# Kernel optimization log

Measured on AMD Instinct MI355X. Metric: run time of the kernel, lower is better.

## Reference

```python
import jax, jax.numpy as jnp
import numpy as np

B, T, L = 512, 1024, 48


def setup_inputs() -> dict:
    key = jax.random.key(0)
    k_e, k_tr, k_st, k_en = jax.random.split(key, 4)
    emissions = jax.random.normal(k_e, (B, T, L), dtype=jnp.float32)
    mask = jnp.ones((B, T), dtype=bool)  # unused by the original decode body
    transitions = jax.random.normal(k_tr, (L, L), dtype=jnp.float32) * 0.1
    start_transitions = jax.random.normal(k_st, (L,), dtype=jnp.float32) * 0.1
    end_transitions = jax.random.normal(k_en, (L,), dtype=jnp.float32) * 0.1
    return {
        "emissions": emissions,
        "mask": mask,
        "transitions": transitions,
        "start_transitions": start_transitions,
        "end_transitions": end_transitions,
    }


def reference(emissions, mask, transitions, start_transitions, end_transitions):
    # Viterbi forward (max-plus recurrence) over time, vectorized over batch.
    v0 = start_transitions[None, :] + emissions[:, 0]  # [B, L]

    def step(v, e_t):
        # scores[b, i, j] = v[b, i] + transitions[i, j]
        scores = v[:, :, None] + transitions[None, :, :]  # [B, L, L]
        best = jnp.max(scores, axis=1)                    # [B, L]
        bp = jnp.argmax(scores, axis=1).astype(jnp.int32)  # [B, L] best prev tag
        return best + e_t, bp

    em_rest = jnp.moveaxis(emissions[:, 1:], 1, 0)  # [T-1, B, L]
    v_final, bps = jax.lax.scan(step, v0, em_rest)  # bps: [T-1, B, L]
    v_final = v_final + end_transitions[None, :]
    best_last = jnp.argmax(v_final, axis=1).astype(jnp.int32)  # [B]

    # Backtrack: bps[t] maps tag at time t+1 -> best tag at time t.
    def back(tag, bp):
        prev = jnp.take_along_axis(bp, tag[:, None], axis=1)[:, 0]  # [B]
        return prev, prev

    _, tags_0_to_Tm2 = jax.lax.scan(back, best_last, bps, reverse=True)  # [T-1, B]
    paths = jnp.concatenate([tags_0_to_Tm2, best_last[None, :]], axis=0)  # [T, B]
    return paths.T  # [B, T] decoded tag sequences
```

## Files before the change

### kernel.cpp

```cpp
#include <hip/hip_runtime.h>
#include <math.h>

#define BB 512
#define TT 1024
#define LL 48
#define PF 8

__device__ __forceinline__ float readlane_f(float v, int lane) {
    return __int_as_float(__builtin_amdgcn_readlane(__float_as_int(v), lane));
}

__device__ __forceinline__ void argmax48(const float* s, float& bestv, int& besti) {
    float val[24];
    int   idx[24];
#pragma unroll
    for (int k = 0; k < 24; ++k) {
        bool c = s[2 * k + 1] > s[2 * k];
        val[k] = c ? s[2 * k + 1] : s[2 * k];
        idx[k] = c ? 2 * k + 1 : 2 * k;
    }
#pragma unroll
    for (int k = 0; k < 12; ++k) {
        bool c = val[2 * k + 1] > val[2 * k];
        val[k] = c ? val[2 * k + 1] : val[2 * k];
        idx[k] = c ? idx[2 * k + 1] : idx[2 * k];
    }
#pragma unroll
    for (int k = 0; k < 6; ++k) {
        bool c = val[2 * k + 1] > val[2 * k];
        val[k] = c ? val[2 * k + 1] : val[2 * k];
        idx[k] = c ? idx[2 * k + 1] : idx[2 * k];
    }
#pragma unroll
    for (int k = 0; k < 3; ++k) {
        bool c = val[2 * k + 1] > val[2 * k];
        val[k] = c ? val[2 * k + 1] : val[2 * k];
        idx[k] = c ? idx[2 * k + 1] : idx[2 * k];
    }
    bool c01 = val[1] > val[0];
    float bv = c01 ? val[1] : val[0];
    int   bi = c01 ? idx[1] : idx[0];
    bool c2 = val[2] > bv;
    bestv = c2 ? val[2] : bv;
    besti = c2 ? idx[2] : bi;
}

__global__ __launch_bounds__(64) void viterbi_kernel(
    const float* __restrict__ emissions,
    const float* __restrict__ transitions,
    const float* __restrict__ start_tr,
    const float* __restrict__ end_tr,
    int* __restrict__ out)
{
    __shared__ unsigned char bp[(TT - 1) * LL];

    const int b  = blockIdx.x;
    const int j  = threadIdx.x;
    const int jc = (j < LL) ? j : (LL - 1);

    float tc[LL];
#pragma unroll
    for (int i = 0; i < LL; ++i)
        tc[i] = transitions[i * LL + jc];

    const float* em = emissions + (size_t)b * TT * LL;

    float v = start_tr[jc] + em[jc];

    float er[PF];
#pragma unroll
    for (int k = 0; k < PF; ++k)
        er[k] = em[(size_t)(1 + k) * LL + jc];

    auto step = [&](int t, float e) {
        float s[LL];
#pragma unroll
        for (int i = 0; i < LL; ++i)
            s[i] = readlane_f(v, i) + tc[i];

        float m1[16];
#pragma unroll
        for (int k = 0; k < 16; ++k)
            m1[k] = fmaxf(fmaxf(s[3 * k], s[3 * k + 1]), s[3 * k + 2]);
        float m2[6];
#pragma unroll
        for (int k = 0; k < 5; ++k)
            m2[k] = fmaxf(fmaxf(m1[3 * k], m1[3 * k + 1]), m1[3 * k + 2]);
        m2[5] = m1[15];
        float best = fmaxf(fmaxf(fmaxf(m2[0], m2[1]), m2[2]),
                           fmaxf(fmaxf(m2[3], m2[4]), m2[5]));

        v = best + e;

        int i0 = 63, i1 = 63, i2 = 63, i3 = 63;
#pragma unroll
        for (int k = 11; k >= 0; --k) {
            if (s[k]      == best) i0 = k;
            if (s[12 + k] == best) i1 = 12 + k;
            if (s[24 + k] == best) i2 = 24 + k;
            if (s[36 + k] == best) i3 = 36 + k;
        }
        int arg = min(min(i0, i1), min(i2, i3));

        bp[(t - 1) * LL + jc] = (unsigned char)arg;
    };

    int tb = 1;
    for (; tb + PF <= TT; tb += PF) {
#pragma unroll
        for (int k = 0; k < PF; ++k) {
            int t = tb + k;
            float e = er[k];
            int tn = t + PF; if (tn > TT - 1) tn = TT - 1;
            er[k] = em[(size_t)tn * LL + jc];
            step(t, e);
        }
    }
#pragma unroll
    for (int k = 0; k < PF - 1; ++k) {
        int t = tb + k;
        if (t < TT) step(t, er[k]);
    }

    v += end_tr[jc];
    float sf[LL];
#pragma unroll
    for (int i = 0; i < LL; ++i)
        sf[i] = readlane_f(v, i);
    float bestv; int tag;
    argmax48(sf, bestv, tag);

    int* ob = out + (size_t)b * TT;
    if (j == 0) ob[TT - 1] = tag;

    for (int hi = TT - 2; hi >= 0; hi -= 32) {
        int lo = hi - 31; if (lo < 0) lo = 0;
        int n = hi - lo + 1;

        unsigned int row[32];
#pragma unroll
        for (int k = 0; k < 32; ++k)
            row[k] = (unsigned int)bp[(lo + k) * LL + jc];

        int outv = 0;
#pragma unroll
        for (int k = 31; k >= 0; --k) {
            if (k < n) {
                tag = __builtin_amdgcn_readlane((int)row[k], tag);
                outv = (j == k) ? tag : outv;
            }
        }
        if (j < n) ob[lo + j] = outv;
    }
}

extern "C" void kernel_launch(void* const* d_in, const int* in_sizes, int n_in,
                              void* d_out, int out_size, void* d_ws, size_t ws_size,
                              hipStream_t stream) {
    const float* emissions   = (const float*)d_in[0];
    const float* transitions = (const float*)d_in[2];
    const float* start_tr    = (const float*)d_in[3];
    const float* end_tr      = (const float*)d_in[4];
    int* out = (int*)d_out;

    viterbi_kernel<<<dim3(BB), dim3(64), 0, stream>>>(
        emissions, transitions, start_tr, end_tr, out);
}
```

Baseline: 572.1 us.

## Process two batch rows per wavefront to interleave independent Viterbi recurrences

Each 64-thread block now decodes two sequences at once, interleaving their max-plus steps and backtracking. The aim is instruction-level parallelism, hiding readlane and dependency latency along the serial time chain. The cost is half as many blocks and twice the instructions per wave. Shared memory for backpointers doubles and is now dynamic, with the max size raised once on the host.

```diff
diff --git a/kernel.cpp b/kernel.cpp
--- a/kernel.cpp
+++ b/kernel.cpp
@@ -45,16 +45,19 @@
     besti = c2 ? idx[2] : bi;
 }
 
-__global__ __launch_bounds__(64) void viterbi_kernel(
+__global__ __launch_bounds__(64, 1) void viterbi_kernel(
     const float* __restrict__ emissions,
     const float* __restrict__ transitions,
     const float* __restrict__ start_tr,
     const float* __restrict__ end_tr,
     int* __restrict__ out)
 {
-    __shared__ unsigned char bp[(TT - 1) * LL];
-
-    const int b  = blockIdx.x;
+    extern __shared__ unsigned char bp[];
+    unsigned char* bpA = bp;
+    unsigned char* bpB = bp + (TT - 1) * LL;
+
+    const int bA = blockIdx.x * 2;
+    const int bB = bA + 1;
     const int j  = threadIdx.x;
     const int jc = (j < LL) ? j : (LL - 1);
 
@@ -63,46 +66,67 @@
     for (int i = 0; i < LL; ++i)
         tc[i] = transitions[i * LL + jc];
 
-    const float* em = emissions + (size_t)b * TT * LL;
-
-    float v = start_tr[jc] + em[jc];
-
-    float er[PF];
-#pragma unroll
-    for (int k = 0; k < PF; ++k)
-        er[k] = em[(size_t)(1 + k) * LL + jc];
-
-    auto step = [&](int t, float e) {
-        float s[LL];
-#pragma unroll
-        for (int i = 0; i < LL; ++i)
-            s[i] = readlane_f(v, i) + tc[i];
-
-        float m1[16];
-#pragma unroll
-        for (int k = 0; k < 16; ++k)
-            m1[k] = fmaxf(fmaxf(s[3 * k], s[3 * k + 1]), s[3 * k + 2]);
-        float m2[6];
-#pragma unroll
-        for (int k = 0; k < 5; ++k)
-            m2[k] = fmaxf(fmaxf(m1[3 * k], m1[3 * k + 1]), m1[3 * k + 2]);
-        m2[5] = m1[15];
-        float best = fmaxf(fmaxf(fmaxf(m2[0], m2[1]), m2[2]),
-                           fmaxf(fmaxf(m2[3], m2[4]), m2[5]));
-
-        v = best + e;
-
-        int i0 = 63, i1 = 63, i2 = 63, i3 = 63;
+    const float* emA = emissions + (size_t)bA * TT * LL;
+    const float* emB = emissions + (size_t)bB * TT * LL;
+
+    float vA = start_tr[jc] + emA[jc];
+    float vB = start_tr[jc] + emB[jc];
+
+    float erA[PF], erB[PF];
+#pragma unroll
+    for (int k = 0; k < PF; ++k) {
+        erA[k] = emA[(size_t)(1 + k) * LL + jc];
+        erB[k] = emB[(size_t)(1 + k) * LL + jc];
+    }
+
+    auto step2 = [&](int t, float eA, float eB) {
+        float sA[LL], sB[LL];
+#pragma unroll
+        for (int i = 0; i < LL; ++i) {
+            sA[i] = readlane_f(vA, i) + tc[i];
+            sB[i] = readlane_f(vB, i) + tc[i];
+        }
+
+        float m1A[16], m1B[16];
+#pragma unroll
+        for (int k = 0; k < 16; ++k) {
+            m1A[k] = fmaxf(fmaxf(sA[3 * k], sA[3 * k + 1]), sA[3 * k + 2]);
+            m1B[k] = fmaxf(fmaxf(sB[3 * k], sB[3 * k + 1]), sB[3 * k + 2]);
+        }
+        float m2A[6], m2B[6];
+#pragma unroll
+        for (int k = 0; k < 5; ++k) {
+            m2A[k] = fmaxf(fmaxf(m1A[3 * k], m1A[3 * k + 1]), m1A[3 * k + 2]);
+            m2B[k] = fmaxf(fmaxf(m1B[3 * k], m1B[3 * k + 1]), m1B[3 * k + 2]);
+        }
+        m2A[5] = m1A[15];
+        m2B[5] = m1B[15];
+        float bestA = fmaxf(fmaxf(fmaxf(m2A[0], m2A[1]), m2A[2]),
+                            fmaxf(fmaxf(m2A[3], m2A[4]), m2A[5]));
+        float bestB = fmaxf(fmaxf(fmaxf(m2B[0], m2B[1]), m2B[2]),
+                            fmaxf(fmaxf(m2B[3], m2B[4]), m2B[5]));
+
+        vA = bestA + eA;
+        vB = bestB + eB;
+
+        int a0 = 63, a1 = 63, a2 = 63, a3 = 63;
+        int b0 = 63, b1 = 63, b2 = 63, b3 = 63;
 #pragma unroll
         for (int k = 11; k >= 0; --k) {
-            if (s[k]      == best) i0 = k;
-            if (s[12 + k] == best) i1 = 12 + k;
-            if (s[24 + k] == best) i2 = 24 + k;
-            if (s[36 + k] == best) i3 = 36 + k;
-        }
-        int arg = min(min(i0, i1), min(i2, i3));
-
-        bp[(t - 1) * LL + jc] = (unsigned char)arg;
+            if (sA[k]      == bestA) a0 = k;
+            if (sA[12 + k] == bestA) a1 = 12 + k;
+            if (sA[24 + k] == bestA) a2 = 24 + k;
+            if (sA[36 + k] == bestA) a3 = 36 + k;
+            if (sB[k]      == bestB) b0 = k;
+            if (sB[12 + k] == bestB) b1 = 12 + k;
+            if (sB[24 + k] == bestB) b2 = 24 + k;
+            if (sB[36 + k] == bestB) b3 = 36 + k;
+        }
+        int argA = min(min(a0, a1), min(a2, a3));
+        int argB = min(min(b0, b1), min(b2, b3));
+
+        bpA[(t - 1) * LL + jc] = (unsigned char)argA;
+        bpB[(t - 1) * LL + jc] = (unsigned char)argB;
     };
 
     int tb = 1;
@@ -110,47 +134,64 @@
 #pragma unroll
         for (int k = 0; k < PF; ++k) {
             int t = tb + k;
-            float e = er[k];
+            float eA = erA[k];
+            float eB = erB[k];
             int tn = t + PF; if (tn > TT - 1) tn = TT - 1;
-            er[k] = em[(size_t)tn * LL + jc];
-            step(t, e);
+            erA[k] = emA[(size_t)tn * LL + jc];
+            erB[k] = emB[(size_t)tn * LL + jc];
+            step2(t, eA, eB);
         }
     }
 #pragma unroll
     for (int k = 0; k < PF - 1; ++k) {
         int t = tb + k;
-        if (t < TT) step(t, er[k]);
-    }
-
-    v += end_tr[jc];
-    float sf[LL];
-#pragma unroll
-    for (int i = 0; i < LL; ++i)
-        sf[i] = readlane_f(v, i);
-    float bestv; int tag;
-    argmax48(sf, bestv, tag);
-
-    int* ob = out + (size_t)b * TT;
-    if (j == 0) ob[TT - 1] = tag;
+        if (t < TT) step2(t, erA[k], erB[k]);
+    }
+
+    vA += end_tr[jc];
+    vB += end_tr[jc];
+    float sfA[LL], sfB[LL];
+#pragma unroll
+    for (int i = 0; i < LL; ++i) {
+        sfA[i] = readlane_f(vA, i);
+        sfB[i] = readlane_f(vB, i);
+    }
+    float bvA, bvB; int tagA, tagB;
+    argmax48(sfA, bvA, tagA);
+    argmax48(sfB, bvB, tagB);
+
+    int* obA = out + (size_t)bA * TT;
+    int* obB = out + (size_t)bB * TT;
+    if (j == 0) {
+        obA[TT - 1] = tagA;
+        obB[TT - 1] = tagB;
+    }
 
     for (int hi = TT - 2; hi >= 0; hi -= 32) {
         int lo = hi - 31; if (lo < 0) lo = 0;
         int n = hi - lo + 1;
 
-        unsigned int row[32];
-#pragma unroll
-        for (int k = 0; k < 32; ++k)
-            row[k] = (unsigned int)bp[(lo + k) * LL + jc];
-
-        int outv = 0;
+        unsigned int rowA[32], rowB[32];
+#pragma unroll
+        for (int k = 0; k < 32; ++k) {
+            rowA[k] = (unsigned int)bpA[(lo + k) * LL + jc];
+            rowB[k] = (unsigned int)bpB[(lo + k) * LL + jc];
+        }
+
+        int outA = 0, outB = 0;
 #pragma unroll
         for (int k = 31; k >= 0; --k) {
             if (k < n) {
-                tag = __builtin_amdgcn_readlane((int)row[k], tag);
-                outv = (j == k) ? tag : outv;
+                tagA = __builtin_amdgcn_readlane((int)rowA[k], tagA);
+                outA = (j == k) ? tagA : outA;
+                tagB = __builtin_amdgcn_readlane((int)rowB[k], tagB);
+                outB = (j == k) ? tagB : outB;
             }
         }
-        if (j < n) ob[lo + j] = outv;
+        if (j < n) {
+            obA[lo + j] = outA;
+            obB[lo + j] = outB;
+        }
     }
 }
 
@@ -163,6 +204,16 @@
     const float* end_tr      = (const float*)d_in[4];
     int* out = (int*)d_out;
 
-    viterbi_kernel<<<dim3(BB), dim3(64), 0, stream>>>(
+    const int lds_bytes = 2 * (TT - 1) * LL;
+
+    static bool attr_set = false;
+    if (!attr_set) {
+        (void)hipFuncSetAttribute((const void*)viterbi_kernel,
+                                  hipFuncAttributeMaxDynamicSharedMemorySize,
+                                  lds_bytes);
+        attr_set = true;
+    }
+
+    viterbi_kernel<<<dim3(BB / 2), dim3(64), lds_bytes, stream>>>(
         emissions, transitions, start_tr, end_tr, out);
 }
```

Result: slower. 1.520 ms (+165.7%).

## Split Viterbi max-plus reduction across two wavefronts with LDS exchange

Applied to the files above, without the earlier changes.

Each block now uses two wavefronts, each handling half of the 48 previous-state candidates per time step. Partial max/argmax values are exchanged through double-buffered shared memory with a barrier each step, and only the first wave writes backpointers and does the backtrack. The goal is to halve the per-step serial readlane and max work on the critical path, at the cost of a workgroup barrier and an LDS round trip every step.

```diff
diff --git a/kernel.cpp b/kernel.cpp
--- a/kernel.cpp
+++ b/kernel.cpp
@@ -5,6 +5,7 @@
 #define TT 1024
 #define LL 48
 #define PF 8
+#define HALF 24
 
 __device__ __forceinline__ float readlane_f(float v, int lane) {
     return __int_as_float(__builtin_amdgcn_readlane(__float_as_int(v), lane));
@@ -45,7 +46,7 @@
     besti = c2 ? idx[2] : bi;
 }
 
-__global__ __launch_bounds__(64) void viterbi_kernel(
+__global__ __launch_bounds__(128) void viterbi_kernel(
     const float* __restrict__ emissions,
     const float* __restrict__ transitions,
     const float* __restrict__ start_tr,
@@ -53,15 +54,19 @@
     int* __restrict__ out)
 {
     __shared__ unsigned char bp[(TT - 1) * LL];
+    __shared__ uint2 xch[2][2][64];
 
-    const int b  = blockIdx.x;
-    const int j  = threadIdx.x;
-    const int jc = (j < LL) ? j : (LL - 1);
+    const int b   = blockIdx.x;
+    const int tid = threadIdx.x;
+    const int w   = tid >> 6;
+    const int j   = tid & 63;
+    const int jc  = (j < LL) ? j : (LL - 1);
+    const int ibase = w * HALF;
 
-    float tc[LL];
+    float tc[HALF];
 #pragma unroll
-    for (int i = 0; i < LL; ++i)
-        tc[i] = transitions[i * LL + jc];
+    for (int i = 0; i < HALF; ++i)
+        tc[i] = transitions[(ibase + i) * LL + jc];
 
     const float* em = emissions + (size_t)b * TT * LL;
 
@@ -72,37 +77,48 @@
     for (int k = 0; k < PF; ++k)
         er[k] = em[(size_t)(1 + k) * LL + jc];
 
-    auto step = [&](int t, float e) {
-        float s[LL];
+    auto step = [&](int t, float e, int parity) {
+        float s[HALF];
 #pragma unroll
-        for (int i = 0; i < LL; ++i)
-            s[i] = readlane_f(v, i) + tc[i];
+        for (int i = 0; i < HALF; ++i)
+            s[i] = readlane_f(v, ibase + i) + tc[i];
 
-        float m1[16];
+        float m1[8];
 #pragma unroll
-        for (int k = 0; k < 16; ++k)
+        for (int k = 0; k < 8; ++k)
             m1[k] = fmaxf(fmaxf(s[3 * k], s[3 * k + 1]), s[3 * k + 2]);
-        float m2[6];
-#pragma unroll
-        for (int k = 0; k < 5; ++k)
-            m2[k] = fmaxf(fmaxf(m1[3 * k], m1[3 * k + 1]), m1[3 * k + 2]);
-        m2[5] = m1[15];
-        float best = fmaxf(fmaxf(fmaxf(m2[0], m2[1]), m2[2]),
-                           fmaxf(fmaxf(m2[3], m2[4]), m2[5]));
+        float mA = fmaxf(fmaxf(m1[0], m1[1]), m1[2]);
+        float mB = fmaxf(fmaxf(m1[3], m1[4]), m1[5]);
+        float mC = fmaxf(m1[6], m1[7]);
+        float best_own = fmaxf(fmaxf(mA, mB), mC);
 
-        v = best + e;
-
-        int i0 = 63, i1 = 63, i2 = 63, i3 = 63;
+        int i0 = 63, i1 = 63;
 #pragma unroll
         for (int k = 11; k >= 0; --k) {
-            if (s[k]      == best) i0 = k;
-            if (s[12 + k] == best) i1 = 12 + k;
-            if (s[24 + k] == best) i2 = 24 + k;
-            if (s[36 + k] == best) i3 = 36 + k;
+            if (s[k]      == best_own) i0 = ibase + k;
+            if (s[12 + k] == best_own) i1 = ibase + 12 + k;
         }
-        int arg = min(min(i0, i1), min(i2, i3));
+        int arg_own = min(i0, i1);
 
-        bp[(t - 1) * LL + jc] = (unsigned char)arg;
+        xch[parity][w][j] = make_uint2(__float_as_uint(best_own), (unsigned)arg_own);
+        asm volatile("s_waitcnt lgkmcnt(0)" ::: "memory");
+        __builtin_amdgcn_s_barrier();
+        uint2 o = xch[parity][w ^ 1][jc];
+        float m_oth = __uint_as_float(o.x);
+        int   a_oth = (int)o.y;
+
+        float m_low  = (w == 0) ? best_own : m_oth;
+        int   a_low  = (w == 0) ? arg_own  : a_oth;
+        float m_high = (w == 0) ? m_oth    : best_own;
+        int   a_high = (w == 0) ? a_oth    : arg_own;
+        bool  hw_    = m_high > m_low;
+        float bestv  = hw_ ? m_high : m_low;
+        int   barg   = hw_ ? a_high : a_low;
+
+        v = bestv + e;
+
+        if (w == 0)
+            bp[(t - 1) * LL + jc] = (unsigned char)barg;
     };
 
     int tb = 1;
@@ -113,44 +129,46 @@
             float e = er[k];
             int tn = t + PF; if (tn > TT - 1) tn = TT - 1;
             er[k] = em[(size_t)tn * LL + jc];
-            step(t, e);
+            step(t, e, (k + 1) & 1);
         }
     }
 #pragma unroll
     for (int k = 0; k < PF - 1; ++k) {
         int t = tb + k;
-        if (t < TT) step(t, er[k]);
+        if (t < TT) step(t, er[k], (k + 1) & 1);
     }
 
-    v += end_tr[jc];
-    float sf[LL];
+    if (w == 0) {
+        float vf = v + end_tr[jc];
+        float sf[LL];
 #pragma unroll
-    for (int i = 0; i < LL; ++i)
-        sf[i] = readlane_f(v, i);
-    float bestv; int tag;
-    argmax48(sf, bestv, tag);
+        for (int i = 0; i < LL; ++i)
+            sf[i] = readlane_f(vf, i);
+        float bestv; int tag;
+        argmax48(sf, bestv, tag);
 
-    int* ob = out + (size_t)b * TT;
-    if (j == 0) ob[TT - 1] = tag;
+        int* ob = out + (size_t)b * TT;
+        if (j == 0) ob[TT - 1] = tag;
 
-    for (int hi = TT - 2; hi >= 0; hi -= 32) {
-        int lo = hi - 31; if (lo < 0) lo = 0;
-        int n = hi - lo + 1;
+        for (int hi = TT - 2; hi >= 0; hi -= 32) {
+            int lo = hi - 31; if (lo < 0) lo = 0;
+            int n = hi - lo + 1;
 
-        unsigned int row[32];
+            unsigned int row[32];
 #pragma unroll
-        for (int k = 0; k < 32; ++k)
-            row[k] = (unsigned int)bp[(lo + k) * LL + jc];
+            for (int k = 0; k < 32; ++k)
+                row[k] = (unsigned int)bp[(lo + k) * LL + jc];
 
-        int outv = 0;
+            int outv = 0;
 #pragma unroll
-        for (int k = 31; k >= 0; --k) {
-            if (k < n) {
-                tag = __builtin_amdgcn_readlane((int)row[k], tag);
-                outv = (j == k) ? tag : outv;
+            for (int k = 31; k >= 0; --k) {
+                if (k < n) {
+                    tag = __builtin_amdgcn_readlane((int)row[k], tag);
+                    outv = (j == k) ? tag : outv;
+                }
             }
+            if (j < n) ob[lo + j] = outv;
         }
-        if (j < n) ob[lo + j] = outv;
     }
 }
 
@@ -163,6 +181,6 @@
     const float* end_tr      = (const float*)d_in[4];
     int* out = (int*)d_out;
 
-    viterbi_kernel<<<dim3(BB), dim3(64), 0, stream>>>(
+    viterbi_kernel<<<dim3(BB), dim3(128), 0, stream>>>(
         emissions, transitions, start_tr, end_tr, out);
 }
```

After: 924.2 us. 61.6% more time.

## Store Viterbi scores to workspace and recompute argmax during backtrack

Applied to the files above, without the earlier changes.

The forward pass no longer computes a per-step argmax backpointer. It only writes the score vector v for each step to a global workspace. The backtrack recomputes each predecessor with a DPP wave-wide max plus a ballot, reading the transition column from LDS. This takes the 48-way equality-scan argmax off the serial forward critical path, at the cost of a 100 MB global write stream and a serial chain of about 1023 wave reductions per sequence during backtrack.

```diff
diff --git a/kernel.cpp b/kernel.cpp
--- a/kernel.cpp
+++ b/kernel.cpp
@@ -5,44 +5,30 @@
 #define TT 1024
 #define LL 48
 #define PF 8
+#define TSTRIDE 49
 
 __device__ __forceinline__ float readlane_f(float v, int lane) {
     return __int_as_float(__builtin_amdgcn_readlane(__float_as_int(v), lane));
 }
 
-__device__ __forceinline__ void argmax48(const float* s, float& bestv, int& besti) {
-    float val[24];
-    int   idx[24];
-#pragma unroll
-    for (int k = 0; k < 24; ++k) {
-        bool c = s[2 * k + 1] > s[2 * k];
-        val[k] = c ? s[2 * k + 1] : s[2 * k];
-        idx[k] = c ? 2 * k + 1 : 2 * k;
-    }
-#pragma unroll
-    for (int k = 0; k < 12; ++k) {
-        bool c = val[2 * k + 1] > val[2 * k];
-        val[k] = c ? val[2 * k + 1] : val[2 * k];
-        idx[k] = c ? idx[2 * k + 1] : idx[2 * k];
-    }
-#pragma unroll
-    for (int k = 0; k < 6; ++k) {
-        bool c = val[2 * k + 1] > val[2 * k];
-        val[k] = c ? val[2 * k + 1] : val[2 * k];
-        idx[k] = c ? idx[2 * k + 1] : idx[2 * k];
-    }
-#pragma unroll
-    for (int k = 0; k < 3; ++k) {
-        bool c = val[2 * k + 1] > val[2 * k];
-        val[k] = c ? val[2 * k + 1] : val[2 * k];
-        idx[k] = c ? idx[2 * k + 1] : idx[2 * k];
-    }
-    bool c01 = val[1] > val[0];
-    float bv = c01 ? val[1] : val[0];
-    int   bi = c01 ? idx[1] : idx[0];
-    bool c2 = val[2] > bv;
-    bestv = c2 ? val[2] : bv;
-    besti = c2 ? idx[2] : bi;
+template <int CTRL>
+__device__ __forceinline__ float dppmax(float x) {
+    int y = __builtin_amdgcn_update_dpp(__float_as_int(x), __float_as_int(x),
+                                        CTRL, 0xF, 0xF, false);
+    return fmaxf(x, __int_as_float(y));
+}
+
+__device__ __forceinline__ int wave_argmax(float z) {
+    float r = z;
+    r = dppmax<0xB1>(r);
+    r = dppmax<0x4E>(r);
+    r = dppmax<0x141>(r);
+    r = dppmax<0x140>(r);
+    r = dppmax<0x142>(r);
+    r = dppmax<0x143>(r);
+    float m = readlane_f(r, 63);
+    unsigned long long eq = __ballot(z == m);
+    return (int)__builtin_ctzll(eq);
 }
 
 __global__ __launch_bounds__(64) void viterbi_kernel(
@@ -50,9 +36,10 @@
     const float* __restrict__ transitions,
     const float* __restrict__ start_tr,
     const float* __restrict__ end_tr,
-    int* __restrict__ out)
+    int* __restrict__ out,
+    float* __restrict__ vws)
 {
-    __shared__ unsigned char bp[(TT - 1) * LL];
+    __shared__ float tlds[LL * TSTRIDE];
 
     const int b  = blockIdx.x;
     const int j  = threadIdx.x;
@@ -60,12 +47,16 @@
 
     float tc[LL];
 #pragma unroll
-    for (int i = 0; i < LL; ++i)
+    for (int i = 0; i < LL; ++i) {
         tc[i] = transitions[i * LL + jc];
+        tlds[i * TSTRIDE + jc] = tc[i];
+    }
 
     const float* em = emissions + (size_t)b * TT * LL;
+    float* vr_g = vws + (size_t)b * TT * LL;
 
     float v = start_tr[jc] + em[jc];
+    vr_g[jc] = v;
 
     float er[PF];
 #pragma unroll
@@ -91,18 +82,7 @@
                            fmaxf(fmaxf(m2[3], m2[4]), m2[5]));
 
         v = best + e;
-
-        int i0 = 63, i1 = 63, i2 = 63, i3 = 63;
-#pragma unroll
-        for (int k = 11; k >= 0; --k) {
-            if (s[k]      == best) i0 = k;
-            if (s[12 + k] == best) i1 = 12 + k;
-            if (s[24 + k] == best) i2 = 24 + k;
-            if (s[36 + k] == best) i3 = 36 + k;
-        }
-        int arg = min(min(i0, i1), min(i2, i3));
-
-        bp[(t - 1) * LL + jc] = (unsigned char)arg;
+        vr_g[(size_t)t * LL + jc] = v;
     };
 
     int tb = 1;
@@ -122,13 +102,8 @@
         if (t < TT) step(t, er[k]);
     }
 
-    v += end_tr[jc];
-    float sf[LL];
-#pragma unroll
-    for (int i = 0; i < LL; ++i)
-        sf[i] = readlane_f(v, i);
-    float bestv; int tag;
-    argmax48(sf, bestv, tag);
+    float vf = (j < LL) ? (v + end_tr[jc]) : -INFINITY;
+    int tag = wave_argmax(vf);
 
     int* ob = out + (size_t)b * TT;
     if (j == 0) ob[TT - 1] = tag;
@@ -137,16 +112,18 @@
         int lo = hi - 31; if (lo < 0) lo = 0;
         int n = hi - lo + 1;
 
-        unsigned int row[32];
+        float vr[32];
 #pragma unroll
-        for (int k = 0; k < 32; ++k)
-            row[k] = (unsigned int)bp[(lo + k) * LL + jc];
+        for (int k = 31; k >= 0; --k)
+            if (k < n) vr[k] = vr_g[(size_t)(lo + k) * LL + jc];
 
         int outv = 0;
 #pragma unroll
         for (int k = 31; k >= 0; --k) {
             if (k < n) {
-                tag = __builtin_amdgcn_readlane((int)row[k], tag);
+                float tcol = tlds[jc * TSTRIDE + tag];
+                float z = (j < LL) ? (vr[k] + tcol) : -INFINITY;
+                tag = wave_argmax(z);
                 outv = (j == k) ? tag : outv;
             }
         }
@@ -163,6 +140,8 @@
     const float* end_tr      = (const float*)d_in[4];
     int* out = (int*)d_out;
 
+    float* vws = (float*)d_ws;
+
     viterbi_kernel<<<dim3(BB), dim3(64), 0, stream>>>(
-        emissions, transitions, start_tr, end_tr, out);
+        emissions, transitions, start_tr, end_tr, out, vws);
 }
```

Result: faster. 528.9 us (-7.6%).
